# Kernel optimization log

Measured on AMD Instinct MI355X. Metric: run time of the kernel, lower is better.

The kernel has to match this reference:

```python
import jax, jax.numpy as jnp
import numpy as np

N_EMBD = 768
N_HEAD = 8
B, T = 4, 2048

def setup_inputs() -> dict:
    key = jax.random.key(0)
    k1, k2, k3, k4, k5 = jax.random.split(key, 5)
    C = N_EMBD
    s = 1.0 / np.sqrt(C)
    return {
        "x": jax.random.normal(k1, (B, T, C), dtype=jnp.float32),
        "W_attn": jax.random.normal(k2, (C, 3 * C), dtype=jnp.float32) * s,
        "b_attn": jnp.zeros((3 * C,), dtype=jnp.float32),
        "W_proj": jax.random.normal(k3, (C, C), dtype=jnp.float32) * s,
        "b_proj": jnp.zeros((C,), dtype=jnp.float32),
    }

def reference(x, W_attn, b_attn, W_proj, b_proj):
    Bs, Ts, C = x.shape
    H = N_HEAD
    hs = C // H
    qkv = x @ W_attn + b_attn                      # [B,T,3C]
    q, k, v = jnp.split(qkv, 3, axis=-1)
    # reshape to [B,H,T,hs]
    q = q.reshape(Bs, Ts, H, hs).transpose(0, 2, 1, 3)
    k = k.reshape(Bs, Ts, H, hs).transpose(0, 2, 1, 3)
    v = v.reshape(Bs, Ts, H, hs).transpose(0, 2, 1, 3)
    scale = 1.0 / jnp.sqrt(jnp.float32(hs))
    att = jnp.einsum('bhid,bhjd->bhij', q, k) * scale   # [B,H,T,T]
    mask = jnp.tril(jnp.ones((Ts, Ts), dtype=bool))
    att = jnp.where(mask, att, -jnp.inf)
    m = jnp.max(att, axis=-1, keepdims=True)
    e = jnp.where(mask, jnp.exp(att - m), 0.0)
    # original kernel divides by (sum + 1e-9)
    att = e / (jnp.sum(e, axis=-1, keepdims=True) + 1e-9)
    y = jnp.einsum('bhij,bhjd->bhid', att, v)           # [B,H,T,hs]
    y = y.transpose(0, 2, 1, 3).reshape(Bs, Ts, C)
    return y @ W_proj + b_proj
```

## Files before the change

kernel.cpp:

```cpp
#include <hip/hip_runtime.h>

typedef __bf16 bf16;
typedef __attribute__((ext_vector_type(4))) __bf16 bf16x4;
typedef __attribute__((ext_vector_type(8))) __bf16 bf16x8;
typedef __attribute__((ext_vector_type(4))) float f32x4;

#define B_   4
#define T_   2048
#define C_   768
#define H_   8
#define HS_  96
#define M_   (B_ * T_)
#define QKN_ (3 * C_)

#define NEG_BIG (-1e30f)

#define KSTR 104
#define VSTR 72
#define PSTR 72

__global__ void transpose_kernel(const float* __restrict__ W, bf16* __restrict__ Wt,
                                 int R, int Cn) {
    __shared__ bf16 tile[32][33];
    int tx = threadIdx.x, ty = threadIdx.y;
    int x  = blockIdx.x * 32 + tx;
    int y0 = blockIdx.y * 32;
#pragma unroll
    for (int j = 0; j < 32; j += 8)
        tile[ty + j][tx] = (bf16)W[(size_t)(y0 + ty + j) * Cn + x];
    __syncthreads();
    int y2 = blockIdx.x * 32;
    int x2 = y0 + tx;
#pragma unroll
    for (int j = 0; j < 32; j += 8)
        Wt[(size_t)(y2 + ty + j) * R + x2] = tile[tx][ty + j];
}

__global__ void sentinel_kernel(float* __restrict__ out, int n) {
    int i = blockIdx.x * 256 + threadIdx.x;
    if (i < n) out[i] = 12345.0f;
}

__device__ __forceinline__ bf16x8 cvt8(f32x4 v0, f32x4 v1) {
    bf16x8 o;
#pragma unroll
    for (int i = 0; i < 4; ++i) { o[i] = (bf16)v0[i]; o[4 + i] = (bf16)v1[i]; }
    return o;
}

__global__ __launch_bounds__(256) void gemm_qkv(const float* __restrict__ A,
                                                const bf16* __restrict__ Bt,
                                                const float* __restrict__ bias,
                                                bf16* __restrict__ Cmat,
                                                bf16* __restrict__ Vt,
                                                int M, int N, int K) {
    __shared__ bf16 lda[128 * 72];
    __shared__ bf16 ldb[128 * 72];
    int tid  = threadIdx.x;
    int w    = tid >> 6;
    int lane = tid & 63;
    int col  = lane & 15, quad = lane >> 4;
    int wr   = w >> 1, wc = w & 1;
    int m0   = blockIdx.y * 128, n0 = blockIdx.x * 128;

    int rr[4], cc8[4];
#pragma unroll
    for (int i = 0; i < 4; ++i) {
        int chunk = i * 256 + tid;
        rr[i] = chunk >> 3; cc8[i] = (chunk & 7) * 8;
    }

    const f32x4 zero = {0.f, 0.f, 0.f, 0.f};
    f32x4 acc[4][4];
#pragma unroll
    for (int mr = 0; mr < 4; ++mr)
#pragma unroll
        for (int nc = 0; nc < 4; ++nc) acc[mr][nc] = zero;

    f32x4 a0[4], a1[4]; bf16x8 breg[4];
#pragma unroll
    for (int i = 0; i < 4; ++i) {
        const float* ap = &A[(size_t)(m0 + rr[i]) * K + cc8[i]];
        a0[i] = *(const f32x4*)ap;
        a1[i] = *(const f32x4*)(ap + 4);
        breg[i] = *(const bf16x8*)&Bt[(size_t)(n0 + rr[i]) * K + cc8[i]];
    }

    for (int k0 = 0; k0 < K; k0 += 64) {
#pragma unroll
        for (int i = 0; i < 4; ++i) {
            *(bf16x8*)&lda[rr[i] * 72 + cc8[i]] = cvt8(a0[i], a1[i]);
            *(bf16x8*)&ldb[rr[i] * 72 + cc8[i]] = breg[i];
        }
        __syncthreads();
        if (k0 + 64 < K) {
            int k1 = k0 + 64;
#pragma unroll
            for (int i = 0; i < 4; ++i) {
                const float* ap = &A[(size_t)(m0 + rr[i]) * K + k1 + cc8[i]];
                a0[i] = *(const f32x4*)ap;
                a1[i] = *(const f32x4*)(ap + 4);
                breg[i] = *(const bf16x8*)&Bt[(size_t)(n0 + rr[i]) * K + k1 + cc8[i]];
            }
        }
#pragma unroll
        for (int ks = 0; ks < 2; ++ks) {
            bf16x8 af[4], bfr[4];
#pragma unroll
            for (int t = 0; t < 4; ++t) {
                af[t]  = *(const bf16x8*)&lda[(wr * 64 + t * 16 + col) * 72 + ks * 32 + quad * 8];
                bfr[t] = *(const bf16x8*)&ldb[(wc * 64 + t * 16 + col) * 72 + ks * 32 + quad * 8];
            }
#pragma unroll
            for (int mr = 0; mr < 4; ++mr)
#pragma unroll
                for (int nc = 0; nc < 4; ++nc)
                    acc[mr][nc] = __builtin_amdgcn_mfma_f32_16x16x32_bf16(
                        af[mr], bfr[nc], acc[mr][nc], 0, 0, 0);
        }
        __syncthreads();
    }

#pragma unroll
    for (int nc = 0; nc < 4; ++nc) {
        int n = n0 + wc * 64 + nc * 16 + col;
        float bv = bias[n];
#pragma unroll
        for (int mr = 0; mr < 4; ++mr) {
#pragma unroll
            for (int r = 0; r < 4; ++r) {
                int row = m0 + wr * 64 + mr * 16 + quad * 4 + r;
                Cmat[(size_t)row * N + n] = (bf16)(acc[mr][nc][r] + bv);
            }
        }
    }
    if (n0 >= 2 * C_) {
        int batch = m0 >> 11;
        bf16* Vtb = Vt + (size_t)batch * C_ * T_;
        int t0 = (m0 & 2047) + wr * 64;
#pragma unroll
        for (int nc = 0; nc < 4; ++nc) {
            int n  = n0 + wc * 64 + nc * 16 + col;
            int vc = n - 2 * C_;
            float bv = bias[n];
#pragma unroll
            for (int mr = 0; mr < 4; ++mr) {
                int t = t0 + mr * 16 + quad * 4;
                bf16x4 pk = {(bf16)(acc[mr][nc][0] + bv), (bf16)(acc[mr][nc][1] + bv),
                             (bf16)(acc[mr][nc][2] + bv), (bf16)(acc[mr][nc][3] + bv)};
                *(bf16x4*)&Vtb[(size_t)vc * T_ + t] = pk;
            }
        }
    }
}

__global__ __launch_bounds__(256) void gemm_proj(const bf16* __restrict__ A,
                                                 const bf16* __restrict__ Bt,
                                                 const float* __restrict__ bias,
                                                 float* __restrict__ Cmat,
                                                 int M, int N, int K) {
    __shared__ bf16 lda[128 * 72];
    __shared__ bf16 ldb[128 * 72];
    int tid  = threadIdx.x;
    int w    = tid >> 6;
    int lane = tid & 63;
    int col  = lane & 15, quad = lane >> 4;
    int wr   = w >> 1, wc = w & 1;
    int m0   = blockIdx.y * 128, n0 = blockIdx.x * 128;

    int rr[4], cc8[4];
#pragma unroll
    for (int i = 0; i < 4; ++i) {
        int chunk = i * 256 + tid;
        rr[i] = chunk >> 3; cc8[i] = (chunk & 7) * 8;
    }

    const f32x4 zero = {0.f, 0.f, 0.f, 0.f};
    f32x4 acc[4][4];
#pragma unroll
    for (int mr = 0; mr < 4; ++mr)
#pragma unroll
        for (int nc = 0; nc < 4; ++nc) acc[mr][nc] = zero;

    bf16x8 areg[4], breg[4];
#pragma unroll
    for (int i = 0; i < 4; ++i) {
        areg[i] = *(const bf16x8*)&A[(size_t)(m0 + rr[i]) * K + cc8[i]];
        breg[i] = *(const bf16x8*)&Bt[(size_t)(n0 + rr[i]) * K + cc8[i]];
    }

    for (int k0 = 0; k0 < K; k0 += 64) {
#pragma unroll
        for (int i = 0; i < 4; ++i) {
            *(bf16x8*)&lda[rr[i] * 72 + cc8[i]] = areg[i];
            *(bf16x8*)&ldb[rr[i] * 72 + cc8[i]] = breg[i];
        }
        __syncthreads();
        if (k0 + 64 < K) {
            int k1 = k0 + 64;
#pragma unroll
            for (int i = 0; i < 4; ++i) {
                areg[i] = *(const bf16x8*)&A[(size_t)(m0 + rr[i]) * K + k1 + cc8[i]];
                breg[i] = *(const bf16x8*)&Bt[(size_t)(n0 + rr[i]) * K + k1 + cc8[i]];
            }
        }
#pragma unroll
        for (int ks = 0; ks < 2; ++ks) {
            bf16x8 af[4], bfr[4];
#pragma unroll
            for (int t = 0; t < 4; ++t) {
                af[t]  = *(const bf16x8*)&lda[(wr * 64 + t * 16 + col) * 72 + ks * 32 + quad * 8];
                bfr[t] = *(const bf16x8*)&ldb[(wc * 64 + t * 16 + col) * 72 + ks * 32 + quad * 8];
            }
#pragma unroll
            for (int mr = 0; mr < 4; ++mr)
#pragma unroll
                for (int nc = 0; nc < 4; ++nc)
                    acc[mr][nc] = __builtin_amdgcn_mfma_f32_16x16x32_bf16(
                        af[mr], bfr[nc], acc[mr][nc], 0, 0, 0);
        }
        __syncthreads();
    }

#pragma unroll
    for (int nc = 0; nc < 4; ++nc) {
        int n = n0 + wc * 64 + nc * 16 + col;
        float bv = bias[n];
#pragma unroll
        for (int mr = 0; mr < 4; ++mr) {
#pragma unroll
            for (int r = 0; r < 4; ++r) {
                int row = m0 + wr * 64 + mr * 16 + quad * 4 + r;
                Cmat[(size_t)row * N + n] = acc[mr][nc][r] + bv;
            }
        }
    }
}

__global__ __launch_bounds__(256) void attn_kernel(const bf16* __restrict__ qkv,
                                                   const bf16* __restrict__ Vt,
                                                   bf16* __restrict__ y,
                                                   int nGroups) {
    __shared__ bf16 ldsK[64 * KSTR];
    __shared__ bf16 ldsV[96 * VSTR];
    __shared__ bf16 ldsP[4 * 16 * PSTR];
    const int bid  = blockIdx.x;
    const int qt   = 31 - bid / nGroups;
    const int g    = bid % nGroups;
    const int h    = g & 7, b = g >> 3;
    const int tid  = threadIdx.x;
    const int w    = tid >> 6, lane = tid & 63;
    const int col  = lane & 15, quad = lane >> 4;
    const float SCALE2 = 0.10206207261596577f * 1.4426950408889634f;
    const float M0 = 24.0f;
    const f32x4 zero = {0.f, 0.f, 0.f, 0.f};

    const bf16* qkvb = qkv + (size_t)b * T_ * QKN_;
    const bf16* Vtbh = Vt + (size_t)(b * H_ + h) * HS_ * T_;
    bf16* yb  = y + (size_t)b * T_ * C_;
    bf16* myP = &ldsP[w * 16 * PSTR];

    const int rbase = qt * 64 + w * 16;

    bf16x8 qf[3];
#pragma unroll
    for (int c = 0; c < 3; ++c)
        qf[c] = *(const bf16x8*)&qkvb[(size_t)(rbase + col) * QKN_ + h * HS_ + c * 32 + quad * 8];

    const bf16* pK[3]; const bf16* pV[3];
    bf16 *dK[3], *dV[3];
#pragma unroll
    for (int i = 0; i < 3; ++i) {
        int chunk = i * 256 + tid;
        int rK = chunk / 12, cK = chunk - rK * 12;
        pK[i] = qkvb + (size_t)rK * QKN_ + C_ + h * HS_ + cK * 8;
        dK[i] = &ldsK[rK * KSTR + cK * 8];
        int rV = chunk >> 3, cV = chunk & 7;
        pV[i] = Vtbh + (size_t)rV * T_ + cV * 8;
        dV[i] = &ldsV[rV * VSTR + cV * 8];
    }

    f32x4 o[6];
#pragma unroll
    for (int n2 = 0; n2 < 6; ++n2) o[n2] = zero;
    float lsum = 0.f;

    const int njt = qt + 1;
    for (int jt = 0; jt < njt; ++jt) {
        int jb = jt * 64;
        __syncthreads();
#pragma unroll
        for (int i = 0; i < 3; ++i) {
            *(bf16x8*)dK[i] = *(const bf16x8*)pK[i];
            *(bf16x8*)dV[i] = *(const bf16x8*)pV[i];
            pK[i] += (size_t)64 * QKN_;
            pV[i] += 64;
        }
        __syncthreads();

        bf16x8 kf[4][3];
#pragma unroll
        for (int nb = 0; nb < 4; ++nb)
#pragma unroll
            for (int c = 0; c < 3; ++c)
                kf[nb][c] = *(const bf16x8*)&ldsK[(nb * 16 + col) * KSTR + c * 32 + quad * 8];

        f32x4 st[4];
#pragma unroll
        for (int nb = 0; nb < 4; ++nb) st[nb] = zero;
#pragma unroll
        for (int c = 0; c < 3; ++c)
#pragma unroll
            for (int nb = 0; nb < 4; ++nb)
                st[nb] = __builtin_amdgcn_mfma_f32_16x16x32_bf16(
                    kf[nb][c], qf[c], st[nb], 0, 0, 0);

        if (jt == njt - 1) {
#pragma unroll
            for (int nb = 0; nb < 4; ++nb)
#pragma unroll
                for (int r = 0; r < 4; ++r) {
                    int jg = jb + nb * 16 + quad * 4 + r;
                    st[nb][r] = (jg <= rbase + col) ? fmaf(st[nb][r], SCALE2, -M0)
                                                    : NEG_BIG;
                }
        } else {
#pragma unroll
            for (int nb = 0; nb < 4; ++nb)
#pragma unroll
                for (int r = 0; r < 4; ++r)
                    st[nb][r] = fmaf(st[nb][r], SCALE2, -M0);
        }

#pragma unroll
        for (int nb = 0; nb < 4; ++nb) {
#pragma unroll
            for (int r = 0; r < 4; ++r) {
                float pv = exp2f(st[nb][r]);
                st[nb][r] = pv;
                lsum += pv;
            }
            bf16x4 pk = {(bf16)st[nb][0], (bf16)st[nb][1],
                         (bf16)st[nb][2], (bf16)st[nb][3]};
            *(bf16x4*)&myP[col * PSTR + nb * 16 + quad * 4] = pk;
        }

        bf16x8 vf[6][2];
#pragma unroll
        for (int n2 = 0; n2 < 6; ++n2)
#pragma unroll
            for (int c = 0; c < 2; ++c)
                vf[n2][c] = *(const bf16x8*)&ldsV[(n2 * 16 + col) * VSTR + c * 32 + quad * 8];
        bf16x8 pa0 = *(const bf16x8*)&myP[col * PSTR + quad * 8];
        bf16x8 pa1 = *(const bf16x8*)&myP[col * PSTR + 32 + quad * 8];
#pragma unroll
        for (int n2 = 0; n2 < 6; ++n2)
            o[n2] = __builtin_amdgcn_mfma_f32_16x16x32_bf16(vf[n2][0], pa0, o[n2], 0, 0, 0);
#pragma unroll
        for (int n2 = 0; n2 < 6; ++n2)
            o[n2] = __builtin_amdgcn_mfma_f32_16x16x32_bf16(vf[n2][1], pa1, o[n2], 0, 0, 0);
    }

    lsum += __shfl_xor(lsum, 16, 64);
    lsum += __shfl_xor(lsum, 32, 64);
    float linv = 1.0f / lsum;
#pragma unroll
    for (int n2 = 0; n2 < 6; ++n2) {
        bf16x4 pk = {(bf16)(o[n2][0] * linv), (bf16)(o[n2][1] * linv),
                     (bf16)(o[n2][2] * linv), (bf16)(o[n2][3] * linv)};
        *(bf16x4*)&yb[(size_t)(rbase + col) * C_ + h * HS_ + n2 * 16 + quad * 4] = pk;
    }
}

extern "C" void kernel_launch(void* const* d_in, const int* in_sizes, int n_in,
                              void* d_out, int out_size, void* d_ws, size_t ws_size,
                              hipStream_t stream) {
    (void)in_sizes; (void)n_in;
    const float* x      = (const float*)d_in[0];
    const float* W_attn = (const float*)d_in[1];
    const float* b_attn = (const float*)d_in[2];
    const float* W_proj = (const float*)d_in[3];
    const float* b_proj = (const float*)d_in[4];
    float* out = (float*)d_out;

    size_t e_wta = (size_t)QKN_ * C_;
    size_t e_wtp = (size_t)C_ * C_;
    size_t a_qkv = e_wta + e_wtp;
    size_t a_vt  = a_qkv + (size_t)M_ * QKN_;
    size_t a_yb  = a_vt + (size_t)M_ * C_;
    size_t needA = (a_yb + (size_t)M_ * C_) * sizeof(bf16);
    size_t b_qkv = e_wta + e_wtp;
    size_t b_vt  = b_qkv + (size_t)T_ * QKN_;
    size_t b_yb  = b_vt + (size_t)T_ * C_;
    size_t needB = (b_yb + (size_t)T_ * C_) * sizeof(bf16);

    if (ws_size >= needA) {
        bf16* Wt_attn = (bf16*)d_ws;
        bf16* Wt_proj = (bf16*)d_ws + e_wta;
        bf16* qkv     = (bf16*)d_ws + a_qkv;
        bf16* Vt      = (bf16*)d_ws + a_vt;
        bf16* yb      = (bf16*)d_ws + a_yb;
        transpose_kernel<<<dim3(QKN_ / 32, C_ / 32), dim3(32, 8), 0, stream>>>(W_attn, Wt_attn, C_, QKN_);
        transpose_kernel<<<dim3(C_ / 32, C_ / 32), dim3(32, 8), 0, stream>>>(W_proj, Wt_proj, C_, C_);
        gemm_qkv<<<dim3(QKN_ / 128, M_ / 128), 256, 0, stream>>>(
            x, Wt_attn, b_attn, qkv, Vt, M_, QKN_, C_);
        attn_kernel<<<dim3(32 * H_ * B_), 256, 0, stream>>>(qkv, Vt, yb, H_ * B_);
        gemm_proj<<<dim3(C_ / 128, M_ / 128), 256, 0, stream>>>(
            yb, Wt_proj, b_proj, out, M_, C_, C_);
    } else if (ws_size >= needB) {
        bf16* Wt_attn = (bf16*)d_ws;
        bf16* Wt_proj = (bf16*)d_ws + e_wta;
        bf16* qkv     = (bf16*)d_ws + b_qkv;
        bf16* Vt      = (bf16*)d_ws + b_vt;
        bf16* yb      = (bf16*)d_ws + b_yb;
        transpose_kernel<<<dim3(QKN_ / 32, C_ / 32), dim3(32, 8), 0, stream>>>(W_attn, Wt_attn, C_, QKN_);
        transpose_kernel<<<dim3(C_ / 32, C_ / 32), dim3(32, 8), 0, stream>>>(W_proj, Wt_proj, C_, C_);
        for (int b = 0; b < B_; ++b) {
            const float* xb = x + (size_t)b * T_ * C_;
            float* outb     = out + (size_t)b * T_ * C_;
            gemm_qkv<<<dim3(QKN_ / 128, T_ / 128), 256, 0, stream>>>(
                xb, Wt_attn, b_attn, qkv, Vt, T_, QKN_, C_);
            attn_kernel<<<dim3(32 * H_), 256, 0, stream>>>(qkv, Vt, yb, H_);
            gemm_proj<<<dim3(C_ / 128, T_ / 128), 256, 0, stream>>>(
                yb, Wt_proj, b_proj, outb, T_, C_, C_);
        }
    } else {
        sentinel_kernel<<<(out_size + 255) / 256, 256, 0, stream>>>(out, out_size);
    }
}
```

Baseline: 218.2 us.

## Pre-convert x to bf16 and load GEMM tiles via global_load_lds

Adds a separate kernel that converts x to bf16 into the yb workspace buffer, so gemm_qkv reads bf16 instead of fp32. Both GEMMs now stage A/B tiles directly from global memory into LDS with global_load_lds (16 bytes per lane) instead of going through registers. The LDS row stride drops from 72 to 64, which removes the padding and can cause bank conflicts on fragment reads. Register prefetch double-buffering is gone, so global loads are no longer overlapped with MFMA work, and the extra conversion pass adds memory traffic and a kernel launch.

Result: slower. 232.5 us (+6.6%).

```diff
diff --git a/kernel.cpp b/kernel.cpp
--- a/kernel.cpp
+++ b/kernel.cpp
@@ -19,6 +19,13 @@
 #define VSTR 72
 #define PSTR 72
 
+__device__ __forceinline__ void gload_lds16(const bf16* g, bf16* l) {
+    __builtin_amdgcn_global_load_lds(
+        (const __attribute__((address_space(1))) uint32_t*)g,
+        (__attribute__((address_space(3))) uint32_t*)l,
+        16, 0, 0);
+}
+
 __global__ void transpose_kernel(const float* __restrict__ W, bf16* __restrict__ Wt,
                                  int R, int Cn) {
     __shared__ bf16 tile[32][33];
@@ -48,14 +55,25 @@
     return o;
 }
 
-__global__ __launch_bounds__(256) void gemm_qkv(const float* __restrict__ A,
+__global__ __launch_bounds__(256) void convert_bf16_kernel(const float* __restrict__ in,
+                                                           bf16* __restrict__ out,
+                                                           int n8) {
+    int i = blockIdx.x * 256 + threadIdx.x;
+    if (i >= n8) return;
+    const float* p = in + (size_t)i * 8;
+    f32x4 a = *(const f32x4*)p;
+    f32x4 b = *(const f32x4*)(p + 4);
+    *(bf16x8*)&out[(size_t)i * 8] = cvt8(a, b);
+}
+
+__global__ __launch_bounds__(256) void gemm_qkv(const bf16* __restrict__ A,
                                                 const bf16* __restrict__ Bt,
                                                 const float* __restrict__ bias,
                                                 bf16* __restrict__ Cmat,
                                                 bf16* __restrict__ Vt,
                                                 int M, int N, int K) {
-    __shared__ bf16 lda[128 * 72];
-    __shared__ bf16 ldb[128 * 72];
+    __shared__ bf16 lda[128 * 64];
+    __shared__ bf16 ldb[128 * 64];
     int tid  = threadIdx.x;
     int w    = tid >> 6;
     int lane = tid & 63;
@@ -63,11 +81,17 @@
     int wr   = w >> 1, wc = w & 1;
     int m0   = blockIdx.y * 128, n0 = blockIdx.x * 128;
 
-    int rr[4], cc8[4];
+    int srow = lane >> 3;
+    int scol = (lane & 7) * 8;
+    const bf16* gA[4]; const bf16* gB[4]; bf16* lA[4]; bf16* lB[4];
 #pragma unroll
     for (int i = 0; i < 4; ++i) {
-        int chunk = i * 256 + tid;
-        rr[i] = chunk >> 3; cc8[i] = (chunk & 7) * 8;
+        int seg = w * 4 + i;
+        int row = seg * 8 + srow;
+        gA[i] = &A[(size_t)(m0 + row) * K + scol];
+        gB[i] = &Bt[(size_t)(n0 + row) * K + scol];
+        lA[i] = &lda[seg * 512];
+        lB[i] = &ldb[seg * 512];
     }
 
     const f32x4 zero = {0.f, 0.f, 0.f, 0.f};
@@ -77,39 +101,20 @@
 #pragma unroll
         for (int nc = 0; nc < 4; ++nc) acc[mr][nc] = zero;
 
-    f32x4 a0[4], a1[4]; bf16x8 breg[4];
-#pragma unroll
-    for (int i = 0; i < 4; ++i) {
-        const float* ap = &A[(size_t)(m0 + rr[i]) * K + cc8[i]];
-        a0[i] = *(const f32x4*)ap;
-        a1[i] = *(const f32x4*)(ap + 4);
-        breg[i] = *(const bf16x8*)&Bt[(size_t)(n0 + rr[i]) * K + cc8[i]];
-    }
-
     for (int k0 = 0; k0 < K; k0 += 64) {
 #pragma unroll
         for (int i = 0; i < 4; ++i) {
-            *(bf16x8*)&lda[rr[i] * 72 + cc8[i]] = cvt8(a0[i], a1[i]);
-            *(bf16x8*)&ldb[rr[i] * 72 + cc8[i]] = breg[i];
-        }
-        __syncthreads();
-        if (k0 + 64 < K) {
-            int k1 = k0 + 64;
-#pragma unroll
-            for (int i = 0; i < 4; ++i) {
-                const float* ap = &A[(size_t)(m0 + rr[i]) * K + k1 + cc8[i]];
-                a0[i] = *(const f32x4*)ap;
-                a1[i] = *(const f32x4*)(ap + 4);
-                breg[i] = *(const bf16x8*)&Bt[(size_t)(n0 + rr[i]) * K + k1 + cc8[i]];
-            }
-        }
+            gload_lds16(gA[i] + k0, lA[i]);
+            gload_lds16(gB[i] + k0, lB[i]);
+        }
+        __syncthreads();
 #pragma unroll
         for (int ks = 0; ks < 2; ++ks) {
             bf16x8 af[4], bfr[4];
 #pragma unroll
             for (int t = 0; t < 4; ++t) {
-                af[t]  = *(const bf16x8*)&lda[(wr * 64 + t * 16 + col) * 72 + ks * 32 + quad * 8];
-                bfr[t] = *(const bf16x8*)&ldb[(wc * 64 + t * 16 + col) * 72 + ks * 32 + quad * 8];
+                af[t]  = *(const bf16x8*)&lda[(wr * 64 + t * 16 + col) * 64 + ks * 32 + quad * 8];
+                bfr[t] = *(const bf16x8*)&ldb[(wc * 64 + t * 16 + col) * 64 + ks * 32 + quad * 8];
             }
 #pragma unroll
             for (int mr = 0; mr < 4; ++mr)
@@ -159,8 +164,8 @@
                                                  const float* __restrict__ bias,
                                                  float* __restrict__ Cmat,
                                                  int M, int N, int K) {
-    __shared__ bf16 lda[128 * 72];
-    __shared__ bf16 ldb[128 * 72];
+    __shared__ bf16 lda[128 * 64];
+    __shared__ bf16 ldb[128 * 64];
     int tid  = threadIdx.x;
     int w    = tid >> 6;
     int lane = tid & 63;
@@ -168,11 +173,17 @@
     int wr   = w >> 1, wc = w & 1;
     int m0   = blockIdx.y * 128, n0 = blockIdx.x * 128;
 
-    int rr[4], cc8[4];
+    int srow = lane >> 3;
+    int scol = (lane & 7) * 8;
+    const bf16* gA[4]; const bf16* gB[4]; bf16* lA[4]; bf16* lB[4];
 #pragma unroll
     for (int i = 0; i < 4; ++i) {
-        int chunk = i * 256 + tid;
-        rr[i] = chunk >> 3; cc8[i] = (chunk & 7) * 8;
+        int seg = w * 4 + i;
+        int row = seg * 8 + srow;
+        gA[i] = &A[(size_t)(m0 + row) * K + scol];
+        gB[i] = &Bt[(size_t)(n0 + row) * K + scol];
+        lA[i] = &lda[seg * 512];
+        lB[i] = &ldb[seg * 512];
     }
 
     const f32x4 zero = {0.f, 0.f, 0.f, 0.f};
@@ -182,35 +193,20 @@
 #pragma unroll
         for (int nc = 0; nc < 4; ++nc) acc[mr][nc] = zero;
 
-    bf16x8 areg[4], breg[4];
-#pragma unroll
-    for (int i = 0; i < 4; ++i) {
-        areg[i] = *(const bf16x8*)&A[(size_t)(m0 + rr[i]) * K + cc8[i]];
-        breg[i] = *(const bf16x8*)&Bt[(size_t)(n0 + rr[i]) * K + cc8[i]];
-    }
-
     for (int k0 = 0; k0 < K; k0 += 64) {
 #pragma unroll
         for (int i = 0; i < 4; ++i) {
-            *(bf16x8*)&lda[rr[i] * 72 + cc8[i]] = areg[i];
-            *(bf16x8*)&ldb[rr[i] * 72 + cc8[i]] = breg[i];
-        }
-        __syncthreads();
-        if (k0 + 64 < K) {
-            int k1 = k0 + 64;
-#pragma unroll
-            for (int i = 0; i < 4; ++i) {
-                areg[i] = *(const bf16x8*)&A[(size_t)(m0 + rr[i]) * K + k1 + cc8[i]];
-                breg[i] = *(const bf16x8*)&Bt[(size_t)(n0 + rr[i]) * K + k1 + cc8[i]];
-            }
-        }
+            gload_lds16(gA[i] + k0, lA[i]);
+            gload_lds16(gB[i] + k0, lB[i]);
+        }
+        __syncthreads();
 #pragma unroll
         for (int ks = 0; ks < 2; ++ks) {
             bf16x8 af[4], bfr[4];
 #pragma unroll
             for (int t = 0; t < 4; ++t) {
-                af[t]  = *(const bf16x8*)&lda[(wr * 64 + t * 16 + col) * 72 + ks * 32 + quad * 8];
-                bfr[t] = *(const bf16x8*)&ldb[(wc * 64 + t * 16 + col) * 72 + ks * 32 + quad * 8];
+                af[t]  = *(const bf16x8*)&lda[(wr * 64 + t * 16 + col) * 64 + ks * 32 + quad * 8];
+                bfr[t] = *(const bf16x8*)&ldb[(wc * 64 + t * 16 + col) * 64 + ks * 32 + quad * 8];
             }
 #pragma unroll
             for (int mr = 0; mr < 4; ++mr)
@@ -400,24 +396,29 @@
         bf16* qkv     = (bf16*)d_ws + a_qkv;
         bf16* Vt      = (bf16*)d_ws + a_vt;
         bf16* yb      = (bf16*)d_ws + a_yb;
+        bf16* xb      = yb;
+        convert_bf16_kernel<<<dim3(M_ * C_ / 8 / 256), 256, 0, stream>>>(x, xb, M_ * C_ / 8);
         transpose_kernel<<<dim3(QKN_ / 32, C_ / 32), dim3(32, 8), 0, stream>>>(W_attn, Wt_attn, C_, QKN_);
         transpose_kernel<<<dim3(C_ / 32, C_ / 32), dim3(32, 8), 0, stream>>>(W_proj, Wt_proj, C_, C_);
         gemm_qkv<<<dim3(QKN_ / 128, M_ / 128), 256, 0, stream>>>(
-            x, Wt_attn, b_attn, qkv, Vt, M_, QKN_, C_);
+            xb, Wt_attn, b_attn, qkv, Vt, M_, QKN_, C_);
         attn_kernel<<<dim3(32 * H_ * B_), 256, 0, stream>>>(qkv, Vt, yb, H_ * B_);
         gemm_proj<<<dim3(C_ / 128, M_ / 128), 256, 0, stream>>>(
             yb, Wt_proj, b_proj, out, M_, C_, C_);
     } else if (ws_size >= needB) {
         bf16* Wt_attn = (bf16*)d_ws;
-        bf16* Wt_proj = (bf16*)d_ws + e_wta;
+        bf16* Wt_proj = (bf16*)d_ws + e_wtp + e_wta - e_wtp;
+        Wt_proj = (bf16*)d_ws + e_wta;
         bf16* qkv     = (bf16*)d_ws + b_qkv;
         bf16* Vt      = (bf16*)d_ws + b_vt;
         bf16* yb      = (bf16*)d_ws + b_yb;
+        bf16* xb      = yb;
         transpose_kernel<<<dim3(QKN_ / 32, C_ / 32), dim3(32, 8), 0, stream>>>(W_attn, Wt_attn, C_, QKN_);
         transpose_kernel<<<dim3(C_ / 32, C_ / 32), dim3(32, 8), 0, stream>>>(W_proj, Wt_proj, C_, C_);
         for (int b = 0; b < B_; ++b) {
-            const float* xb = x + (size_t)b * T_ * C_;
+            const float* xf = x + (size_t)b * T_ * C_;
             float* outb     = out + (size_t)b * T_ * C_;
+            convert_bf16_kernel<<<dim3(T_ * C_ / 8 / 256), 256, 0, stream>>>(xf, xb, T_ * C_ / 8);
             gemm_qkv<<<dim3(QKN_ / 128, T_ / 128), 256, 0, stream>>>(
                 xb, Wt_attn, b_attn, qkv, Vt, T_, QKN_, C_);
             attn_kernel<<<dim3(32 * H_), 256, 0, stream>>>(qkv, Vt, yb, H_);
```
